# Kernel optimization log

Measured on AMD Instinct MI355X. Metric: run time of the kernel, lower is better.

## Reference

```python
import jax, jax.numpy as jnp
import numpy as np

EXP_CLAMP = 1.0e6
DENOM_EPS = 1e-10
LRELU_ALPHA = 0.01


def setup_inputs() -> dict:
    key = jax.random.key(0)
    k1, k2, k3, k4, k5, k6 = jax.random.split(key, 6)
    B, N, E, F = 4, 16384, 262144, 64
    h = jax.random.normal(k1, (B, N, F), dtype=jnp.float32)
    edge = jax.random.randint(k2, (B, E, 2), 0, N, dtype=jnp.int32)
    edge_num = jax.random.randint(k3, (B,), 1, E, dtype=jnp.int32)
    edge_weight = jax.random.uniform(k4, (B, E), dtype=jnp.float32)
    W = jax.random.normal(k5, (F, F), dtype=jnp.float32) * 0.15  # xavier-ish scale
    a = jax.random.normal(k6, (1, 2 * F), dtype=jnp.float32) * 0.12
    return {"h": h, "edge": edge, "edge_num": edge_num,
            "edge_weight": edge_weight, "W": W, "a": a}


def _seg_sum(src, idx, num_segments):
    # src: [E, ...], idx: [E] -> [num_segments, ...]
    return jax.ops.segment_sum(src, idx, num_segments=num_segments)


def reference(h, edge, edge_num, edge_weight, W, a):
    B, N, Fin = h.shape
    E = edge.shape[1]
    # linear transform: Wh = h @ W^T  -> [B, N, Fout]
    Wh = jnp.einsum('bnf,of->bno', h, W)
    ctr = edge[:, :, 0]  # [B, E]
    nbr = edge[:, :, 1]  # [B, E]
    Wh_c = jnp.take_along_axis(Wh, ctr[:, :, None], axis=1)  # [B, E, Fout]
    Wh_n = jnp.take_along_axis(Wh, nbr[:, :, None], axis=1)  # [B, E, Fout]
    a_input = jnp.concatenate([Wh_c, Wh_n], axis=-1) * edge_weight[:, :, None]
    # attention logits: leakyrelu(a_input @ a^T), squeeze to [B, E]
    att1 = jax.nn.leaky_relu(jnp.einsum('bek,k->be', a_input, a[0]), LRELU_ALPHA)
    # per-batch valid-edge mask (edges beyond edge_num zeroed, as in torch loop)
    mask = (jnp.arange(E, dtype=jnp.int32)[None, :] < edge_num[:, None])
    x_exp = jnp.clip(jnp.exp(att1), 0.0, EXP_CLAMP) * mask.astype(att1.dtype)
    # segment softmax denominator over center nodes
    denom = DENOM_EPS + jax.vmap(_seg_sum, in_axes=(0, 0, None))(x_exp, ctr, N)  # [B, N]
    att = x_exp / jnp.take_along_axis(denom, ctr, axis=1)  # [B, E]
    # weighted neighbor aggregation via scatter-add on center index
    att_Wh = Wh_n * att[:, :, None]  # masked edges already have att == 0
    h_prime = jax.vmap(_seg_sum, in_axes=(0, 0, None))(att_Wh, ctr, N)  # [B, N, Fout]
    return jax.nn.relu(h_prime)
```

## Files before the change

kernel.cpp:

```cpp
#include <hip/hip_runtime.h>

#define BB 4
#define NN 16384
#define EE 262144
#define FF 64
#define ROWS (BB * NN)
#define CAP 64
#define CHUNKS 64
#define CHUNK_E (EE / CHUNKS)
#define TILE_R 256

typedef __bf16 bf16x8 __attribute__((ext_vector_type(8)));
typedef float  f32x4  __attribute__((ext_vector_type(4)));

__device__ __forceinline__ unsigned short f32_to_bf16(float f) {
    unsigned int u = __float_as_uint(f);
    u += 0x7FFFu + ((u >> 16) & 1u);
    return (unsigned short)(u >> 16);
}

__global__ __launch_bounds__(256) void mfma_kernel(
    const float* __restrict__ h, const float* __restrict__ W,
    const float* __restrict__ a,
    unsigned short* __restrict__ Wh,
    float* __restrict__ sc, float* __restrict__ sn)
{
    __shared__ float wc[FF], wn[FF];
    const int t = threadIdx.x;
    const int lane = t & 63;
    const int m = lane & 15;
    const int q = lane >> 4;

    if (t < 128) {
        const int f = t & 63;
        const float* av = a + (t >> 6) * FF;
        float s = 0.0f;
        #pragma unroll 8
        for (int o = 0; o < FF; ++o)
            s = fmaf(av[o], W[o * FF + f], s);
        (t < 64 ? wc : wn)[f] = s;
    }

    bf16x8 bfrag[4][2];
    #pragma unroll
    for (int nt = 0; nt < 4; ++nt) {
        const float* wr = W + (nt * 16 + m) * FF;
        #pragma unroll
        for (int kh = 0; kh < 2; ++kh) {
            const float4 v0 = *(const float4*)(wr + kh * 32 + q * 8);
            const float4 v1 = *(const float4*)(wr + kh * 32 + q * 8 + 4);
            bf16x8 b;
            b[0] = (__bf16)v0.x; b[1] = (__bf16)v0.y;
            b[2] = (__bf16)v0.z; b[3] = (__bf16)v0.w;
            b[4] = (__bf16)v1.x; b[5] = (__bf16)v1.y;
            b[6] = (__bf16)v1.z; b[7] = (__bf16)v1.w;
            bfrag[nt][kh] = b;
        }
    }

    __syncthreads();

    const int waveId = (blockIdx.x * 256 + t) >> 6;
    const int R0 = waveId * 16;
    const float* hr = h + (size_t)(R0 + m) * FF;
    bf16x8 af[2];
    float s1 = 0.0f, s2 = 0.0f;
    #pragma unroll
    for (int kh = 0; kh < 2; ++kh) {
        const float4 v0 = *(const float4*)(hr + kh * 32 + q * 8);
        const float4 v1 = *(const float4*)(hr + kh * 32 + q * 8 + 4);
        bf16x8 aa;
        aa[0] = (__bf16)v0.x; aa[1] = (__bf16)v0.y;
        aa[2] = (__bf16)v0.z; aa[3] = (__bf16)v0.w;
        aa[4] = (__bf16)v1.x; aa[5] = (__bf16)v1.y;
        aa[6] = (__bf16)v1.z; aa[7] = (__bf16)v1.w;
        af[kh] = aa;
        const int fb = kh * 32 + q * 8;
        const float4 c0 = *(const float4*)&wc[fb];
        const float4 c1 = *(const float4*)&wc[fb + 4];
        const float4 n0 = *(const float4*)&wn[fb];
        const float4 n1 = *(const float4*)&wn[fb + 4];
        s1 = fmaf(v0.x, c0.x, fmaf(v0.y, c0.y, fmaf(v0.z, c0.z, fmaf(v0.w, c0.w, s1))));
        s1 = fmaf(v1.x, c1.x, fmaf(v1.y, c1.y, fmaf(v1.z, c1.z, fmaf(v1.w, c1.w, s1))));
        s2 = fmaf(v0.x, n0.x, fmaf(v0.y, n0.y, fmaf(v0.z, n0.z, fmaf(v0.w, n0.w, s2))));
        s2 = fmaf(v1.x, n1.x, fmaf(v1.y, n1.y, fmaf(v1.z, n1.z, fmaf(v1.w, n1.w, s2))));
    }
    s1 += __shfl_xor(s1, 16); s2 += __shfl_xor(s2, 16);
    s1 += __shfl_xor(s1, 32); s2 += __shfl_xor(s2, 32);
    if (lane < 16) { sc[R0 + m] = s1; sn[R0 + m] = s2; }

    #pragma unroll
    for (int nt = 0; nt < 4; ++nt) {
        f32x4 acc = {0.f, 0.f, 0.f, 0.f};
        acc = __builtin_amdgcn_mfma_f32_16x16x32_bf16(af[0], bfrag[nt][0], acc, 0, 0, 0);
        acc = __builtin_amdgcn_mfma_f32_16x16x32_bf16(af[1], bfrag[nt][1], acc, 0, 0, 0);
        #pragma unroll
        for (int i = 0; i < 4; ++i)
            Wh[(size_t)(R0 + q * 4 + i) * FF + nt * 16 + m] = f32_to_bf16(acc[i]);
    }
}

__global__ __launch_bounds__(1024) void hist_kernel(
    const int* __restrict__ edge, const int* __restrict__ edge_num,
    unsigned short* __restrict__ histG)
{
    __shared__ unsigned int hist[NN];
    const int g = blockIdx.x;
    const int b = g >> 6, c = g & (CHUNKS - 1);
    const int t = threadIdx.x;
    const int en = edge_num[b];
    const int e0 = c * CHUNK_E;
    if (e0 >= en) return;

    for (int r = t; r < NN; r += 1024) hist[r] = 0u;
    __syncthreads();

    const int2* ep = (const int2*)edge + (size_t)b * EE + e0;
    const int nAct = min(en - e0, CHUNK_E);
    for (int j = t; j < nAct; j += 1024)
        atomicAdd(&hist[ep[j].x], 1u);
    __syncthreads();

    ushort2* out2 = (ushort2*)(histG + (size_t)g * NN);
    for (int r2 = t; r2 < NN / 2; r2 += 1024) {
        ushort2 v;
        v.x = (unsigned short)hist[2 * r2];
        v.y = (unsigned short)hist[2 * r2 + 1];
        out2[r2] = v;
    }
}

__global__ __launch_bounds__(256) void scan_kernel(
    const int* __restrict__ edge_num,
    unsigned short* __restrict__ histG, int* __restrict__ cnt)
{
    __shared__ unsigned short tile[CHUNKS][TILE_R];
    const int g = blockIdx.x;
    const int b = g >> 6, tl = g & 63;
    const int r0 = tl * TILE_R;
    const int t = threadIdx.x;
    const int en = edge_num[b];
    const int nact = min((en + CHUNK_E - 1) / CHUNK_E, CHUNKS);

    for (int c = 0; c < nact; ++c)
        tile[c][t] = histG[(size_t)(b * CHUNKS + c) * NN + r0 + t];
    __syncthreads();

    unsigned int acc = 0;
    for (int c = 0; c < nact; ++c) {
        const unsigned int v = tile[c][t];
        tile[c][t] = (unsigned short)(acc > 65535u ? 65535u : acc);
        acc += v;
    }
    cnt[b * NN + r0 + t] = (int)acc;

    for (int c = 0; c < nact; ++c)
        histG[(size_t)(b * CHUNKS + c) * NN + r0 + t] = tile[c][t];
}

__global__ __launch_bounds__(1024) void scatter_kernel(
    const int* __restrict__ edge, const int* __restrict__ edge_num,
    const unsigned short* __restrict__ baseG,
    unsigned int* __restrict__ payload)
{
    __shared__ unsigned int slotA[NN];
    const int g = blockIdx.x;
    const int b = g >> 6, c = g & (CHUNKS - 1);
    const int t = threadIdx.x;
    const int en = edge_num[b];
    const int e0 = c * CHUNK_E;
    if (e0 >= en) return;

    const ushort2* b2 = (const ushort2*)(baseG + (size_t)(b * CHUNKS + c) * NN);
    for (int r2 = t; r2 < NN / 2; r2 += 1024) {
        const ushort2 v = b2[r2];
        slotA[2 * r2]     = v.x;
        slotA[2 * r2 + 1] = v.y;
    }
    __syncthreads();

    const int2* ep = (const int2*)edge + (size_t)b * EE + e0;
    const int nAct = min(en - e0, CHUNK_E);
    unsigned int* payB = payload + (size_t)b * NN * CAP;

    for (int j = t; j < nAct; j += 1024) {
        const int2 e2 = ep[j];
        const unsigned int slot = atomicAdd(&slotA[e2.x], 1u);
        const unsigned int eid  = (unsigned int)(e0 + j);
        if (slot < CAP)
            payB[(size_t)e2.x * CAP + slot] = (eid << 14) | (unsigned int)e2.y;
    }
}

__global__ __launch_bounds__(256) void gather_kernel(
    const int* __restrict__ cnt, const unsigned int* __restrict__ payload,
    const uint2* __restrict__ Wh2,
    const float* __restrict__ sc, const float* __restrict__ sn,
    const float* __restrict__ ew,
    float* __restrict__ out)
{
    const int bi = blockIdx.x;
    const int xcd = bi & 7;
    const int batch = xcd >> 1;
    const int within = ((bi >> 3) << 1) | (xcd & 1);
    const int w = threadIdx.x >> 6;
    const int lane = threadIdx.x & 63;
    const int r = lane >> 4;
    const int f = lane & 15;
    const int gbase = lane & 48;
    const int rq = within * 4 + w;
    const int row = batch * NN + rq * 4 + r;

    const unsigned int* pl = payload + (size_t)row * CAP;
    const uint2* WhB = Wh2 + (size_t)batch * NN * 16;
    const float* snB = sn + batch * NN;
    const float* ewB = ew + (size_t)batch * EE;

    int deg = cnt[row];
    unsigned int raw = pl[f];
    const float scr = sc[row];
    if (deg > CAP) deg = CAP;

    int jmax = deg;
    jmax = max(jmax, __shfl_xor(jmax, 16));
    jmax = max(jmax, __shfl_xor(jmax, 32));

    float a0 = 0.f, a1 = 0.f, a2 = 0.f, a3 = 0.f, pdsum = 0.f;

    for (int base = 0; base < jmax; base += 16) {
        unsigned int p = 0u;
        if (base + f < deg) {
            const float s0 = ewB[raw >> 14] * (scr + snB[raw & 0x3FFFu]);
            const float s1v = s0 > 0.0f ? s0 : 0.01f * s0;
            const float xe = fminf(__expf(s1v), 1000000.0f);
            pdsum += xe;
            p = ((__float_as_uint(xe) + 0x2000u) & 0xFFFFC000u) | (raw & 0x3FFFu);
        }
        unsigned int rawN = 0u;
        if (base + 16 < jmax) rawN = pl[base + 16 + f];

        const int lim = min(16, jmax - base);
        for (int j4 = 0; j4 < lim; j4 += 4) {
            const unsigned int pv0 = __shfl(p, gbase + j4 + 0);
            const unsigned int pv1 = __shfl(p, gbase + j4 + 1);
            const unsigned int pv2 = __shfl(p, gbase + j4 + 2);
            const unsigned int pv3 = __shfl(p, gbase + j4 + 3);
            const uint2 w0 = WhB[(size_t)(pv0 & 0x3FFFu) * 16 + f];
            const uint2 w1 = WhB[(size_t)(pv1 & 0x3FFFu) * 16 + f];
            const uint2 w2 = WhB[(size_t)(pv2 & 0x3FFFu) * 16 + f];
            const uint2 w3 = WhB[(size_t)(pv3 & 0x3FFFu) * 16 + f];
            const float xe0 = __uint_as_float(pv0 & 0xFFFFC000u);
            const float xe1 = __uint_as_float(pv1 & 0xFFFFC000u);
            const float xe2 = __uint_as_float(pv2 & 0xFFFFC000u);
            const float xe3 = __uint_as_float(pv3 & 0xFFFFC000u);
            a0 = fmaf(xe0, __uint_as_float(w0.x << 16),         a0);
            a1 = fmaf(xe0, __uint_as_float(w0.x & 0xFFFF0000u), a1);
            a2 = fmaf(xe0, __uint_as_float(w0.y << 16),         a2);
            a3 = fmaf(xe0, __uint_as_float(w0.y & 0xFFFF0000u), a3);
            a0 = fmaf(xe1, __uint_as_float(w1.x << 16),         a0);
            a1 = fmaf(xe1, __uint_as_float(w1.x & 0xFFFF0000u), a1);
            a2 = fmaf(xe1, __uint_as_float(w1.y << 16),         a2);
            a3 = fmaf(xe1, __uint_as_float(w1.y & 0xFFFF0000u), a3);
            a0 = fmaf(xe2, __uint_as_float(w2.x << 16),         a0);
            a1 = fmaf(xe2, __uint_as_float(w2.x & 0xFFFF0000u), a1);
            a2 = fmaf(xe2, __uint_as_float(w2.y << 16),         a2);
            a3 = fmaf(xe2, __uint_as_float(w2.y & 0xFFFF0000u), a3);
            a0 = fmaf(xe3, __uint_as_float(w3.x << 16),         a0);
            a1 = fmaf(xe3, __uint_as_float(w3.x & 0xFFFF0000u), a1);
            a2 = fmaf(xe3, __uint_as_float(w3.y << 16),         a2);
            a3 = fmaf(xe3, __uint_as_float(w3.y & 0xFFFF0000u), a3);
        }
        raw = rawN;
    }

    pdsum += __shfl_xor(pdsum, 1);
    pdsum += __shfl_xor(pdsum, 2);
    pdsum += __shfl_xor(pdsum, 4);
    pdsum += __shfl_xor(pdsum, 8);

    const float inv = 1.0f / (1e-10f + pdsum);
    float4 o;
    o.x = fmaxf(a0 * inv, 0.0f);
    o.y = fmaxf(a1 * inv, 0.0f);
    o.z = fmaxf(a2 * inv, 0.0f);
    o.w = fmaxf(a3 * inv, 0.0f);
    ((float4*)out)[(size_t)row * 16 + f] = o;
}

extern "C" void kernel_launch(void* const* d_in, const int* in_sizes, int n_in,
                              void* d_out, int out_size, void* d_ws, size_t ws_size,
                              hipStream_t stream)
{
    const float* h        = (const float*)d_in[0];
    const int*   edge     = (const int*)  d_in[1];
    const int*   edge_num = (const int*)  d_in[2];
    const float* ew       = (const float*)d_in[3];
    const float* W        = (const float*)d_in[4];
    const float* a        = (const float*)d_in[5];
    float* out = (float*)d_out;

    unsigned short* Wh = (unsigned short*)d_ws;
    float* sc        = (float*)(Wh + (size_t)BB * NN * FF);
    float* sn        = sc + ROWS;
    int*   cnt       = (int*)(sn + ROWS);
    unsigned int* payload = (unsigned int*)(cnt + ROWS);
    unsigned short* histG = (unsigned short*)(payload + (size_t)ROWS * CAP);

    mfma_kernel<<<1024, 256, 0, stream>>>(h, W, a, Wh, sc, sn);

    hist_kernel<<<BB * CHUNKS, 1024, 0, stream>>>(edge, edge_num, histG);

    scan_kernel<<<BB * (NN / TILE_R), 256, 0, stream>>>(edge_num, histG, cnt);

    scatter_kernel<<<BB * CHUNKS, 1024, 0, stream>>>(edge, edge_num,
                                                     histG, payload);

    gather_kernel<<<4096, 256, 0, stream>>>(cnt, payload,
                                            (const uint2*)Wh,
                                            sc, sn, ew, out);
}
```

Baseline: 134.0 us.

## Fuse MFMA transform with histogram and scan with scatter to cut launches

Merges the bf16 MFMA linear-transform kernel and the per-chunk histogram kernel into one 256-block kernel of 1024 threads. It also removes the separate scan kernel: each scatter block now sums the histograms of all earlier chunks to find its base offsets, and the last chunk writes the per-node counts. This removes two kernel launches and the scan's read-write round trip through global memory. In exchange, later chunks reread up to 63 histogram slices, so redundant global reads grow with chunk index. The scan also no longer clamps offsets at 65535.

```diff
diff --git a/kernel.cpp b/kernel.cpp
--- a/kernel.cpp
+++ b/kernel.cpp
@@ -8,7 +8,6 @@
 #define CAP 64
 #define CHUNKS 64
 #define CHUNK_E (EE / CHUNKS)
-#define TILE_R 256
 
 typedef __bf16 bf16x8 __attribute__((ext_vector_type(8)));
 typedef float  f32x4  __attribute__((ext_vector_type(4)));
@@ -19,13 +18,16 @@
     return (unsigned short)(u >> 16);
 }
 
-__global__ __launch_bounds__(256) void mfma_kernel(
+__global__ __launch_bounds__(1024) void mfma_hist_kernel(
     const float* __restrict__ h, const float* __restrict__ W,
     const float* __restrict__ a,
+    const int* __restrict__ edge, const int* __restrict__ edge_num,
     unsigned short* __restrict__ Wh,
-    float* __restrict__ sc, float* __restrict__ sn)
+    float* __restrict__ sc, float* __restrict__ sn,
+    unsigned short* __restrict__ histG)
 {
     __shared__ float wc[FF], wn[FF];
+    __shared__ unsigned int hist[NN];
     const int t = threadIdx.x;
     const int lane = t & 63;
     const int m = lane & 15;
@@ -60,108 +62,75 @@
 
     __syncthreads();
 
-    const int waveId = (blockIdx.x * 256 + t) >> 6;
-    const int R0 = waveId * 16;
-    const float* hr = h + (size_t)(R0 + m) * FF;
-    bf16x8 af[2];
-    float s1 = 0.0f, s2 = 0.0f;
-    #pragma unroll
-    for (int kh = 0; kh < 2; ++kh) {
-        const float4 v0 = *(const float4*)(hr + kh * 32 + q * 8);
-        const float4 v1 = *(const float4*)(hr + kh * 32 + q * 8 + 4);
-        bf16x8 aa;
-        aa[0] = (__bf16)v0.x; aa[1] = (__bf16)v0.y;
-        aa[2] = (__bf16)v0.z; aa[3] = (__bf16)v0.w;
-        aa[4] = (__bf16)v1.x; aa[5] = (__bf16)v1.y;
-        aa[6] = (__bf16)v1.z; aa[7] = (__bf16)v1.w;
-        af[kh] = aa;
-        const int fb = kh * 32 + q * 8;
-        const float4 c0 = *(const float4*)&wc[fb];
-        const float4 c1 = *(const float4*)&wc[fb + 4];
-        const float4 n0 = *(const float4*)&wn[fb];
-        const float4 n1 = *(const float4*)&wn[fb + 4];
-        s1 = fmaf(v0.x, c0.x, fmaf(v0.y, c0.y, fmaf(v0.z, c0.z, fmaf(v0.w, c0.w, s1))));
-        s1 = fmaf(v1.x, c1.x, fmaf(v1.y, c1.y, fmaf(v1.z, c1.z, fmaf(v1.w, c1.w, s1))));
-        s2 = fmaf(v0.x, n0.x, fmaf(v0.y, n0.y, fmaf(v0.z, n0.z, fmaf(v0.w, n0.w, s2))));
-        s2 = fmaf(v1.x, n1.x, fmaf(v1.y, n1.y, fmaf(v1.z, n1.z, fmaf(v1.w, n1.w, s2))));
-    }
-    s1 += __shfl_xor(s1, 16); s2 += __shfl_xor(s2, 16);
-    s1 += __shfl_xor(s1, 32); s2 += __shfl_xor(s2, 32);
-    if (lane < 16) { sc[R0 + m] = s1; sn[R0 + m] = s2; }
-
-    #pragma unroll
-    for (int nt = 0; nt < 4; ++nt) {
-        f32x4 acc = {0.f, 0.f, 0.f, 0.f};
-        acc = __builtin_amdgcn_mfma_f32_16x16x32_bf16(af[0], bfrag[nt][0], acc, 0, 0, 0);
-        acc = __builtin_amdgcn_mfma_f32_16x16x32_bf16(af[1], bfrag[nt][1], acc, 0, 0, 0);
+    {
+        const int waveId = blockIdx.x * 16 + (t >> 6);
+        const int R0 = waveId * 16;
+        const float* hr = h + (size_t)(R0 + m) * FF;
+        bf16x8 af[2];
+        float s1 = 0.0f, s2 = 0.0f;
         #pragma unroll
-        for (int i = 0; i < 4; ++i)
-            Wh[(size_t)(R0 + q * 4 + i) * FF + nt * 16 + m] = f32_to_bf16(acc[i]);
-    }
-}
-
-__global__ __launch_bounds__(1024) void hist_kernel(
-    const int* __restrict__ edge, const int* __restrict__ edge_num,
-    unsigned short* __restrict__ histG)
-{
-    __shared__ unsigned int hist[NN];
+        for (int kh = 0; kh < 2; ++kh) {
+            const float4 v0 = *(const float4*)(hr + kh * 32 + q * 8);
+            const float4 v1 = *(const float4*)(hr + kh * 32 + q * 8 + 4);
+            bf16x8 aa;
+            aa[0] = (__bf16)v0.x; aa[1] = (__bf16)v0.y;
+            aa[2] = (__bf16)v0.z; aa[3] = (__bf16)v0.w;
+            aa[4] = (__bf16)v1.x; aa[5] = (__bf16)v1.y;
+            aa[6] = (__bf16)v1.z; aa[7] = (__bf16)v1.w;
+            af[kh] = aa;
+            const int fb = kh * 32 + q * 8;
+            const float4 c0 = *(const float4*)&wc[fb];
+            const float4 c1 = *(const float4*)&wc[fb + 4];
+            const float4 n0 = *(const float4*)&wn[fb];
+            const float4 n1 = *(const float4*)&wn[fb + 4];
+            s1 = fmaf(v0.x, c0.x, fmaf(v0.y, c0.y, fmaf(v0.z, c0.z, fmaf(v0.w, c0.w, s1))));
+            s1 = fmaf(v1.x, c1.x, fmaf(v1.y, c1.y, fmaf(v1.z, c1.z, fmaf(v1.w, c1.w, s1))));
+            s2 = fmaf(v0.x, n0.x, fmaf(v0.y, n0.y, fmaf(v0.z, n0.z, fmaf(v0.w, n0.w, s2))));
+            s2 = fmaf(v1.x, n1.x, fmaf(v1.y, n1.y, fmaf(v1.z, n1.z, fmaf(v1.w, n1.w, s2))));
+        }
+        s1 += __shfl_xor(s1, 16); s2 += __shfl_xor(s2, 16);
+        s1 += __shfl_xor(s1, 32); s2 += __shfl_xor(s2, 32);
+        if (lane < 16) { sc[R0 + m] = s1; sn[R0 + m] = s2; }
+
+        #pragma unroll
+        for (int nt = 0; nt < 4; ++nt) {
+            f32x4 acc = {0.f, 0.f, 0.f, 0.f};
+            acc = __builtin_amdgcn_mfma_f32_16x16x32_bf16(af[0], bfrag[nt][0], acc, 0, 0, 0);
+            acc = __builtin_amdgcn_mfma_f32_16x16x32_bf16(af[1], bfrag[nt][1], acc, 0, 0, 0);
+            #pragma unroll
+            for (int i = 0; i < 4; ++i)
+                Wh[(size_t)(R0 + q * 4 + i) * FF + nt * 16 + m] = f32_to_bf16(acc[i]);
+        }
+    }
+
     const int g = blockIdx.x;
     const int b = g >> 6, c = g & (CHUNKS - 1);
-    const int t = threadIdx.x;
     const int en = edge_num[b];
     const int e0 = c * CHUNK_E;
-    if (e0 >= en) return;
-
-    for (int r = t; r < NN; r += 1024) hist[r] = 0u;
-    __syncthreads();
-
-    const int2* ep = (const int2*)edge + (size_t)b * EE + e0;
-    const int nAct = min(en - e0, CHUNK_E);
-    for (int j = t; j < nAct; j += 1024)
-        atomicAdd(&hist[ep[j].x], 1u);
-    __syncthreads();
-
-    ushort2* out2 = (ushort2*)(histG + (size_t)g * NN);
-    for (int r2 = t; r2 < NN / 2; r2 += 1024) {
-        ushort2 v;
-        v.x = (unsigned short)hist[2 * r2];
-        v.y = (unsigned short)hist[2 * r2 + 1];
-        out2[r2] = v;
-    }
-}
-
-__global__ __launch_bounds__(256) void scan_kernel(
-    const int* __restrict__ edge_num,
-    unsigned short* __restrict__ histG, int* __restrict__ cnt)
-{
-    __shared__ unsigned short tile[CHUNKS][TILE_R];
-    const int g = blockIdx.x;
-    const int b = g >> 6, tl = g & 63;
-    const int r0 = tl * TILE_R;
-    const int t = threadIdx.x;
-    const int en = edge_num[b];
-    const int nact = min((en + CHUNK_E - 1) / CHUNK_E, CHUNKS);
-
-    for (int c = 0; c < nact; ++c)
-        tile[c][t] = histG[(size_t)(b * CHUNKS + c) * NN + r0 + t];
-    __syncthreads();
-
-    unsigned int acc = 0;
-    for (int c = 0; c < nact; ++c) {
-        const unsigned int v = tile[c][t];
-        tile[c][t] = (unsigned short)(acc > 65535u ? 65535u : acc);
-        acc += v;
-    }
-    cnt[b * NN + r0 + t] = (int)acc;
-
-    for (int c = 0; c < nact; ++c)
-        histG[(size_t)(b * CHUNKS + c) * NN + r0 + t] = tile[c][t];
-}
-
-__global__ __launch_bounds__(1024) void scatter_kernel(
+    if (e0 < en) {
+        for (int r = t; r < NN; r += 1024) hist[r] = 0u;
+        __syncthreads();
+
+        const int2* ep = (const int2*)edge + (size_t)b * EE + e0;
+        const int nAct = min(en - e0, CHUNK_E);
+        for (int j = t; j < nAct; j += 1024)
+            atomicAdd(&hist[ep[j].x], 1u);
+        __syncthreads();
+
+        ushort2* out2 = (ushort2*)(histG + (size_t)g * NN);
+        for (int r2 = t; r2 < NN / 2; r2 += 1024) {
+            ushort2 v;
+            v.x = (unsigned short)hist[2 * r2];
+            v.y = (unsigned short)hist[2 * r2 + 1];
+            out2[r2] = v;
+        }
+    }
+}
+
+__global__ __launch_bounds__(1024) void scan_scatter_kernel(
     const int* __restrict__ edge, const int* __restrict__ edge_num,
-    const unsigned short* __restrict__ baseG,
-    unsigned int* __restrict__ payload)
+    const unsigned short* __restrict__ histG,
+    int* __restrict__ cnt, unsigned int* __restrict__ payload)
 {
     __shared__ unsigned int slotA[NN];
     const int g = blockIdx.x;
@@ -170,12 +139,51 @@
     const int en = edge_num[b];
     const int e0 = c * CHUNK_E;
     if (e0 >= en) return;
-
-    const ushort2* b2 = (const ushort2*)(baseG + (size_t)(b * CHUNKS + c) * NN);
-    for (int r2 = t; r2 < NN / 2; r2 += 1024) {
-        const ushort2 v = b2[r2];
-        slotA[2 * r2]     = v.x;
-        slotA[2 * r2 + 1] = v.y;
+    const int nact = min((en + CHUNK_E - 1) / CHUNK_E, CHUNKS);
+    const bool last = (c == nact - 1);
+
+    const unsigned short* hb = histG + (size_t)(b * CHUNKS) * NN;
+    unsigned int ax0 = 0, ay0 = 0, ax1 = 0, ay1 = 0, ax2 = 0, ay2 = 0, ax3 = 0, ay3 = 0;
+    unsigned int ax4 = 0, ay4 = 0, ax5 = 0, ay5 = 0, ax6 = 0, ay6 = 0, ax7 = 0, ay7 = 0;
+    for (int cc = 0; cc < c; ++cc) {
+        const ushort2* hc = (const ushort2*)(hb + (size_t)cc * NN);
+        const ushort2 v0 = hc[t];           ax0 += v0.x; ay0 += v0.y;
+        const ushort2 v1 = hc[t + 1024];    ax1 += v1.x; ay1 += v1.y;
+        const ushort2 v2 = hc[t + 2048];    ax2 += v2.x; ay2 += v2.y;
+        const ushort2 v3 = hc[t + 3072];    ax3 += v3.x; ay3 += v3.y;
+        const ushort2 v4 = hc[t + 4096];    ax4 += v4.x; ay4 += v4.y;
+        const ushort2 v5 = hc[t + 5120];    ax5 += v5.x; ay5 += v5.y;
+        const ushort2 v6 = hc[t + 6144];    ax6 += v6.x; ay6 += v6.y;
+        const ushort2 v7 = hc[t + 7168];    ax7 += v7.x; ay7 += v7.y;
+    }
+    slotA[2 * t]            = ax0; slotA[2 * t + 1]            = ay0;
+    slotA[2 * (t + 1024)]   = ax1; slotA[2 * (t + 1024) + 1]   = ay1;
+    slotA[2 * (t + 2048)]   = ax2; slotA[2 * (t + 2048) + 1]   = ay2;
+    slotA[2 * (t + 3072)]   = ax3; slotA[2 * (t + 3072) + 1]   = ay3;
+    slotA[2 * (t + 4096)]   = ax4; slotA[2 * (t + 4096) + 1]   = ay4;
+    slotA[2 * (t + 5120)]   = ax5; slotA[2 * (t + 5120) + 1]   = ay5;
+    slotA[2 * (t + 6144)]   = ax6; slotA[2 * (t + 6144) + 1]   = ay6;
+    slotA[2 * (t + 7168)]   = ax7; slotA[2 * (t + 7168) + 1]   = ay7;
+
+    if (last) {
+        const ushort2* hc = (const ushort2*)(hb + (size_t)c * NN);
+        int* cb = cnt + b * NN;
+        const ushort2 w0 = hc[t];
+        cb[2 * t]     = (int)(ax0 + w0.x); cb[2 * t + 1]     = (int)(ay0 + w0.y);
+        const ushort2 w1 = hc[t + 1024];
+        cb[2 * (t + 1024)]     = (int)(ax1 + w1.x); cb[2 * (t + 1024) + 1]     = (int)(ay1 + w1.y);
+        const ushort2 w2 = hc[t + 2048];
+        cb[2 * (t + 2048)]     = (int)(ax2 + w2.x); cb[2 * (t + 2048) + 1]     = (int)(ay2 + w2.y);
+        const ushort2 w3 = hc[t + 3072];
+        cb[2 * (t + 3072)]     = (int)(ax3 + w3.x); cb[2 * (t + 3072) + 1]     = (int)(ay3 + w3.y);
+        const ushort2 w4 = hc[t + 4096];
+        cb[2 * (t + 4096)]     = (int)(ax4 + w4.x); cb[2 * (t + 4096) + 1]     = (int)(ay4 + w4.y);
+        const ushort2 w5 = hc[t + 5120];
+        cb[2 * (t + 5120)]     = (int)(ax5 + w5.x); cb[2 * (t + 5120) + 1]     = (int)(ay5 + w5.y);
+        const ushort2 w6 = hc[t + 6144];
+        cb[2 * (t + 6144)]     = (int)(ax6 + w6.x); cb[2 * (t + 6144) + 1]     = (int)(ay6 + w6.y);
+        const ushort2 w7 = hc[t + 7168];
+        cb[2 * (t + 7168)]     = (int)(ax7 + w7.x); cb[2 * (t + 7168) + 1]     = (int)(ay7 + w7.y);
     }
     __syncthreads();
 
@@ -306,14 +314,11 @@
     unsigned int* payload = (unsigned int*)(cnt + ROWS);
     unsigned short* histG = (unsigned short*)(payload + (size_t)ROWS * CAP);
 
-    mfma_kernel<<<1024, 256, 0, stream>>>(h, W, a, Wh, sc, sn);
-
-    hist_kernel<<<BB * CHUNKS, 1024, 0, stream>>>(edge, edge_num, histG);
-
-    scan_kernel<<<BB * (NN / TILE_R), 256, 0, stream>>>(edge_num, histG, cnt);
-
-    scatter_kernel<<<BB * CHUNKS, 1024, 0, stream>>>(edge, edge_num,
-                                                     histG, payload);
+    mfma_hist_kernel<<<256, 1024, 0, stream>>>(h, W, a, edge, edge_num,
+                                               Wh, sc, sn, histG);
+
+    scan_scatter_kernel<<<256, 1024, 0, stream>>>(edge, edge_num, histG,
+                                                  cnt, payload);
 
     gather_kernel<<<4096, 256, 0, stream>>>(cnt, payload,
                                             (const uint2*)Wh,
```

After: 141.6 us. 5.7% more time.

## Fuse matmul, histogram, scan and scatter into one cooperative kernel

Applied to the files above, without the earlier changes.

The MFMA projection, per-chunk histogram, chunk prefix scan and payload scatter now run in a single cooperative kernel of 256 blocks with 1024 threads, separated by grid-wide syncs, instead of four separate launches. The scan phase is re-split so each block uses 1024 threads over four quarter-ranges of chunks with a small cross-quarter prefix. The goal is to remove launch gaps and tail effects between the small kernels. The cost is grid.sync overhead, less parallelism in the matmul and scan phases (fewer, larger blocks), and a dependence on all 256 blocks being co-resident.

```diff
diff --git a/kernel.cpp b/kernel.cpp
--- a/kernel.cpp
+++ b/kernel.cpp
@@ -1,4 +1,7 @@
 #include <hip/hip_runtime.h>
+#include <hip/hip_cooperative_groups.h>
+
+namespace cg = cooperative_groups;
 
 #define BB 4
 #define NN 16384
@@ -19,13 +22,20 @@
     return (unsigned short)(u >> 16);
 }
 
-__global__ __launch_bounds__(256) void mfma_kernel(
+__global__ __launch_bounds__(1024) void mega_kernel(
     const float* __restrict__ h, const float* __restrict__ W,
     const float* __restrict__ a,
+    const int* __restrict__ edge, const int* __restrict__ edge_num,
     unsigned short* __restrict__ Wh,
-    float* __restrict__ sc, float* __restrict__ sn)
+    float* __restrict__ sc, float* __restrict__ sn,
+    unsigned short* __restrict__ histG,
+    int* __restrict__ cnt, unsigned int* __restrict__ payload)
 {
     __shared__ float wc[FF], wn[FF];
+    __shared__ unsigned int shm[NN];
+    cg::grid_group grid = cg::this_grid();
+
+    const int blk = blockIdx.x;
     const int t = threadIdx.x;
     const int lane = t & 63;
     const int m = lane & 15;
@@ -57,138 +67,140 @@
             bfrag[nt][kh] = b;
         }
     }
-
     __syncthreads();
 
-    const int waveId = (blockIdx.x * 256 + t) >> 6;
-    const int R0 = waveId * 16;
-    const float* hr = h + (size_t)(R0 + m) * FF;
-    bf16x8 af[2];
-    float s1 = 0.0f, s2 = 0.0f;
-    #pragma unroll
-    for (int kh = 0; kh < 2; ++kh) {
-        const float4 v0 = *(const float4*)(hr + kh * 32 + q * 8);
-        const float4 v1 = *(const float4*)(hr + kh * 32 + q * 8 + 4);
-        bf16x8 aa;
-        aa[0] = (__bf16)v0.x; aa[1] = (__bf16)v0.y;
-        aa[2] = (__bf16)v0.z; aa[3] = (__bf16)v0.w;
-        aa[4] = (__bf16)v1.x; aa[5] = (__bf16)v1.y;
-        aa[6] = (__bf16)v1.z; aa[7] = (__bf16)v1.w;
-        af[kh] = aa;
-        const int fb = kh * 32 + q * 8;
-        const float4 c0 = *(const float4*)&wc[fb];
-        const float4 c1 = *(const float4*)&wc[fb + 4];
-        const float4 n0 = *(const float4*)&wn[fb];
-        const float4 n1 = *(const float4*)&wn[fb + 4];
-        s1 = fmaf(v0.x, c0.x, fmaf(v0.y, c0.y, fmaf(v0.z, c0.z, fmaf(v0.w, c0.w, s1))));
-        s1 = fmaf(v1.x, c1.x, fmaf(v1.y, c1.y, fmaf(v1.z, c1.z, fmaf(v1.w, c1.w, s1))));
-        s2 = fmaf(v0.x, n0.x, fmaf(v0.y, n0.y, fmaf(v0.z, n0.z, fmaf(v0.w, n0.w, s2))));
-        s2 = fmaf(v1.x, n1.x, fmaf(v1.y, n1.y, fmaf(v1.z, n1.z, fmaf(v1.w, n1.w, s2))));
-    }
-    s1 += __shfl_xor(s1, 16); s2 += __shfl_xor(s2, 16);
-    s1 += __shfl_xor(s1, 32); s2 += __shfl_xor(s2, 32);
-    if (lane < 16) { sc[R0 + m] = s1; sn[R0 + m] = s2; }
-
-    #pragma unroll
-    for (int nt = 0; nt < 4; ++nt) {
-        f32x4 acc = {0.f, 0.f, 0.f, 0.f};
-        acc = __builtin_amdgcn_mfma_f32_16x16x32_bf16(af[0], bfrag[nt][0], acc, 0, 0, 0);
-        acc = __builtin_amdgcn_mfma_f32_16x16x32_bf16(af[1], bfrag[nt][1], acc, 0, 0, 0);
+    {
+        const int waveId = blk * 16 + (t >> 6);
+        const int R0 = waveId * 16;
+        const float* hr = h + (size_t)(R0 + m) * FF;
+        bf16x8 af[2];
+        float s1 = 0.0f, s2 = 0.0f;
         #pragma unroll
-        for (int i = 0; i < 4; ++i)
-            Wh[(size_t)(R0 + q * 4 + i) * FF + nt * 16 + m] = f32_to_bf16(acc[i]);
-    }
-}
-
-__global__ __launch_bounds__(1024) void hist_kernel(
-    const int* __restrict__ edge, const int* __restrict__ edge_num,
-    unsigned short* __restrict__ histG)
-{
-    __shared__ unsigned int hist[NN];
-    const int g = blockIdx.x;
-    const int b = g >> 6, c = g & (CHUNKS - 1);
-    const int t = threadIdx.x;
-    const int en = edge_num[b];
-    const int e0 = c * CHUNK_E;
-    if (e0 >= en) return;
-
-    for (int r = t; r < NN; r += 1024) hist[r] = 0u;
-    __syncthreads();
-
-    const int2* ep = (const int2*)edge + (size_t)b * EE + e0;
-    const int nAct = min(en - e0, CHUNK_E);
-    for (int j = t; j < nAct; j += 1024)
-        atomicAdd(&hist[ep[j].x], 1u);
-    __syncthreads();
-
-    ushort2* out2 = (ushort2*)(histG + (size_t)g * NN);
-    for (int r2 = t; r2 < NN / 2; r2 += 1024) {
-        ushort2 v;
-        v.x = (unsigned short)hist[2 * r2];
-        v.y = (unsigned short)hist[2 * r2 + 1];
-        out2[r2] = v;
-    }
-}
-
-__global__ __launch_bounds__(256) void scan_kernel(
-    const int* __restrict__ edge_num,
-    unsigned short* __restrict__ histG, int* __restrict__ cnt)
-{
-    __shared__ unsigned short tile[CHUNKS][TILE_R];
-    const int g = blockIdx.x;
-    const int b = g >> 6, tl = g & 63;
-    const int r0 = tl * TILE_R;
-    const int t = threadIdx.x;
-    const int en = edge_num[b];
-    const int nact = min((en + CHUNK_E - 1) / CHUNK_E, CHUNKS);
-
-    for (int c = 0; c < nact; ++c)
-        tile[c][t] = histG[(size_t)(b * CHUNKS + c) * NN + r0 + t];
-    __syncthreads();
-
-    unsigned int acc = 0;
-    for (int c = 0; c < nact; ++c) {
-        const unsigned int v = tile[c][t];
-        tile[c][t] = (unsigned short)(acc > 65535u ? 65535u : acc);
-        acc += v;
-    }
-    cnt[b * NN + r0 + t] = (int)acc;
-
-    for (int c = 0; c < nact; ++c)
-        histG[(size_t)(b * CHUNKS + c) * NN + r0 + t] = tile[c][t];
-}
-
-__global__ __launch_bounds__(1024) void scatter_kernel(
-    const int* __restrict__ edge, const int* __restrict__ edge_num,
-    const unsigned short* __restrict__ baseG,
-    unsigned int* __restrict__ payload)
-{
-    __shared__ unsigned int slotA[NN];
-    const int g = blockIdx.x;
-    const int b = g >> 6, c = g & (CHUNKS - 1);
-    const int t = threadIdx.x;
-    const int en = edge_num[b];
-    const int e0 = c * CHUNK_E;
-    if (e0 >= en) return;
-
-    const ushort2* b2 = (const ushort2*)(baseG + (size_t)(b * CHUNKS + c) * NN);
-    for (int r2 = t; r2 < NN / 2; r2 += 1024) {
-        const ushort2 v = b2[r2];
-        slotA[2 * r2]     = v.x;
-        slotA[2 * r2 + 1] = v.y;
-    }
-    __syncthreads();
-
-    const int2* ep = (const int2*)edge + (size_t)b * EE + e0;
-    const int nAct = min(en - e0, CHUNK_E);
-    unsigned int* payB = payload + (size_t)b * NN * CAP;
-
-    for (int j = t; j < nAct; j += 1024) {
-        const int2 e2 = ep[j];
-        const unsigned int slot = atomicAdd(&slotA[e2.x], 1u);
-        const unsigned int eid  = (unsigned int)(e0 + j);
-        if (slot < CAP)
-            payB[(size_t)e2.x * CAP + slot] = (eid << 14) | (unsigned int)e2.y;
+        for (int kh = 0; kh < 2; ++kh) {
+            const float4 v0 = *(const float4*)(hr + kh * 32 + q * 8);
+            const float4 v1 = *(const float4*)(hr + kh * 32 + q * 8 + 4);
+            bf16x8 aa;
+            aa[0] = (__bf16)v0.x; aa[1] = (__bf16)v0.y;
+            aa[2] = (__bf16)v0.z; aa[3] = (__bf16)v0.w;
+            aa[4] = (__bf16)v1.x; aa[5] = (__bf16)v1.y;
+            aa[6] = (__bf16)v1.z; aa[7] = (__bf16)v1.w;
+            af[kh] = aa;
+            const int fb = kh * 32 + q * 8;
+            const float4 c0 = *(const float4*)&wc[fb];
+            const float4 c1 = *(const float4*)&wc[fb + 4];
+            const float4 n0 = *(const float4*)&wn[fb];
+            const float4 n1 = *(const float4*)&wn[fb + 4];
+            s1 = fmaf(v0.x, c0.x, fmaf(v0.y, c0.y, fmaf(v0.z, c0.z, fmaf(v0.w, c0.w, s1))));
+            s1 = fmaf(v1.x, c1.x, fmaf(v1.y, c1.y, fmaf(v1.z, c1.z, fmaf(v1.w, c1.w, s1))));
+            s2 = fmaf(v0.x, n0.x, fmaf(v0.y, n0.y, fmaf(v0.z, n0.z, fmaf(v0.w, n0.w, s2))));
+            s2 = fmaf(v1.x, n1.x, fmaf(v1.y, n1.y, fmaf(v1.z, n1.z, fmaf(v1.w, n1.w, s2))));
+        }
+        s1 += __shfl_xor(s1, 16); s2 += __shfl_xor(s2, 16);
+        s1 += __shfl_xor(s1, 32); s2 += __shfl_xor(s2, 32);
+        if (lane < 16) { sc[R0 + m] = s1; sn[R0 + m] = s2; }
+
+        #pragma unroll
+        for (int nt = 0; nt < 4; ++nt) {
+            f32x4 acc = {0.f, 0.f, 0.f, 0.f};
+            acc = __builtin_amdgcn_mfma_f32_16x16x32_bf16(af[0], bfrag[nt][0], acc, 0, 0, 0);
+            acc = __builtin_amdgcn_mfma_f32_16x16x32_bf16(af[1], bfrag[nt][1], acc, 0, 0, 0);
+            #pragma unroll
+            for (int i = 0; i < 4; ++i)
+                Wh[(size_t)(R0 + q * 4 + i) * FF + nt * 16 + m] = f32_to_bf16(acc[i]);
+        }
+    }
+
+    {
+        const int b = blk >> 6, c = blk & (CHUNKS - 1);
+        const int en = edge_num[b];
+        const int e0 = c * CHUNK_E;
+        if (e0 < en) {
+            for (int r = t; r < NN; r += 1024) shm[r] = 0u;
+            __syncthreads();
+            const int2* ep = (const int2*)edge + (size_t)b * EE + e0;
+            const int nAct = min(en - e0, CHUNK_E);
+            for (int j = t; j < nAct; j += 1024)
+                atomicAdd(&shm[ep[j].x], 1u);
+            __syncthreads();
+            ushort2* out2 = (ushort2*)(histG + (size_t)blk * NN);
+            for (int r2 = t; r2 < NN / 2; r2 += 1024) {
+                ushort2 v;
+                v.x = (unsigned short)shm[2 * r2];
+                v.y = (unsigned short)shm[2 * r2 + 1];
+                out2[r2] = v;
+            }
+        }
+    }
+
+    __threadfence();
+    grid.sync();
+
+    {
+        const int b = blk >> 6, tl = blk & 63;
+        const int r0 = tl * TILE_R;
+        const int rr = t & 255;
+        const int qt = t >> 8;
+        const int en = edge_num[b];
+        const int nact = min((en + CHUNK_E - 1) / CHUNK_E, CHUNKS);
+
+        unsigned short* tile = (unsigned short*)shm;
+        unsigned int* qs = (unsigned int*)(tile + CHUNKS * TILE_R);
+
+        const unsigned short* hb = histG + (size_t)(b * CHUNKS) * NN + r0;
+        unsigned int s = 0;
+        #pragma unroll 4
+        for (int c = qt * 16; c < qt * 16 + 16; ++c) {
+            const unsigned int v = (c < nact) ? (unsigned int)hb[(size_t)c * NN + rr] : 0u;
+            tile[c * TILE_R + rr] = (unsigned short)v;
+            s += v;
+        }
+        qs[qt * TILE_R + rr] = s;
+        __syncthreads();
+
+        unsigned int acc = 0;
+        for (int qq = 0; qq < 3; ++qq)
+            if (qq < qt) acc += qs[qq * TILE_R + rr];
+        #pragma unroll 4
+        for (int c = qt * 16; c < qt * 16 + 16; ++c) {
+            const unsigned int v = tile[c * TILE_R + rr];
+            tile[c * TILE_R + rr] = (unsigned short)(acc > 65535u ? 65535u : acc);
+            acc += v;
+        }
+        if (qt == 3) cnt[b * NN + r0 + rr] = (int)acc;
+        __syncthreads();
+
+        unsigned short* hbw = histG + (size_t)(b * CHUNKS) * NN + r0;
+        #pragma unroll 4
+        for (int c = qt * 16; c < qt * 16 + 16; ++c)
+            if (c < nact) hbw[(size_t)c * NN + rr] = tile[c * TILE_R + rr];
+    }
+
+    __threadfence();
+    grid.sync();
+
+    {
+        const int b = blk >> 6, c = blk & (CHUNKS - 1);
+        const int en = edge_num[b];
+        const int e0 = c * CHUNK_E;
+        if (e0 < en) {
+            const ushort2* b2 = (const ushort2*)(histG + (size_t)(b * CHUNKS + c) * NN);
+            for (int r2 = t; r2 < NN / 2; r2 += 1024) {
+                const ushort2 v = b2[r2];
+                shm[2 * r2]     = v.x;
+                shm[2 * r2 + 1] = v.y;
+            }
+            __syncthreads();
+            const int2* ep = (const int2*)edge + (size_t)b * EE + e0;
+            const int nAct = min(en - e0, CHUNK_E);
+            unsigned int* payB = payload + (size_t)b * NN * CAP;
+            for (int j = t; j < nAct; j += 1024) {
+                const int2 e2 = ep[j];
+                const unsigned int slot = atomicAdd(&shm[e2.x], 1u);
+                const unsigned int eid  = (unsigned int)(e0 + j);
+                if (slot < CAP)
+                    payB[(size_t)e2.x * CAP + slot] = (eid << 14) | (unsigned int)e2.y;
+            }
+        }
     }
 }
 
@@ -306,14 +318,11 @@
     unsigned int* payload = (unsigned int*)(cnt + ROWS);
     unsigned short* histG = (unsigned short*)(payload + (size_t)ROWS * CAP);
 
-    mfma_kernel<<<1024, 256, 0, stream>>>(h, W, a, Wh, sc, sn);
-
-    hist_kernel<<<BB * CHUNKS, 1024, 0, stream>>>(edge, edge_num, histG);
-
-    scan_kernel<<<BB * (NN / TILE_R), 256, 0, stream>>>(edge_num, histG, cnt);
-
-    scatter_kernel<<<BB * CHUNKS, 1024, 0, stream>>>(edge, edge_num,
-                                                     histG, payload);
+    void* args[] = { (void*)&h, (void*)&W, (void*)&a, (void*)&edge,
+                     (void*)&edge_num, (void*)&Wh, (void*)&sc, (void*)&sn,
+                     (void*)&histG, (void*)&cnt, (void*)&payload };
+    hipLaunchCooperativeKernel((const void*)mega_kernel, dim3(256), dim3(1024),
+                               args, 0, stream);
 
     gather_kernel<<<4096, 256, 0, stream>>>(cnt, payload,
                                             (const uint2*)Wh,
```

New measurement: 388.4 us. 190% more time.
